# Kernel optimization log

Measured on AMD Instinct MI355X. Metric: run time of the kernel, lower is better.

The kernel has to match this reference:

```python
import jax, jax.numpy as jnp
import numpy as np

N_GRAPH = 1024
NODES_PER_GRAPH = 512
TOTAL_NODES = N_GRAPH * NODES_PER_GRAPH  # 524288
D_FEAT = 128
EPS = 1e-06


def setup_inputs() -> dict:
    key = jax.random.key(0)
    k1, k2, k3, k4 = jax.random.split(key, 4)
    x = jax.random.normal(k1, (TOTAL_NODES, D_FEAT), dtype=jnp.float32)
    # per-graph node counts; sum(n_node) == TOTAL_NODES (equal-size graphs)
    n_node = jnp.full((N_GRAPH,), NODES_PER_GRAPH, dtype=jnp.int32)
    mean_scale = jax.random.uniform(k2, (D_FEAT,), dtype=jnp.float32)
    scale = jax.random.uniform(k3, (D_FEAT,), dtype=jnp.float32)
    bias = jax.random.normal(k4, (D_FEAT,), dtype=jnp.float32)
    return {"x": x, "n_node": n_node, "mean_scale": mean_scale, "scale": scale, "bias": bias}


def reference(x, n_node, mean_scale, scale, bias):
    n_graph = n_node.shape[0]
    total_nodes = x.shape[0]
    node_graph_idx = jnp.repeat(jnp.arange(n_graph), n_node, axis=0,
                                total_repeat_length=total_nodes)  # [N]
    ones = jnp.ones((total_nodes, 1), dtype=x.dtype)
    counts = jax.ops.segment_sum(ones, node_graph_idx, n_graph)  # [G,1]
    # per-graph mean, broadcast back to nodes
    mean_g = jax.ops.segment_sum(x, node_graph_idx, n_graph) / counts  # [G,D]
    mean_n = jnp.repeat(mean_g, n_node, axis=0, total_repeat_length=total_nodes)
    # NOTE: faithful to source - the mean is scaled by mean_scale BEFORE both
    # the centering and the variance computation.
    mean_n = mean_n * mean_scale
    y = x - mean_n
    var_g = jax.ops.segment_sum((x - mean_n) ** 2, node_graph_idx, n_graph) / counts
    var_n = jnp.repeat(var_g, n_node, axis=0, total_repeat_length=total_nodes)
    mul = jax.lax.rsqrt(var_n + EPS) * scale
    y = y * mul + bias
    return y.astype(x.dtype)
```

## Files before the change

### kernel.cpp

```cpp
#include <hip/hip_runtime.h>

#define D_FEAT 128
#define F4 (D_FEAT / 4)
#define BLOCK 512
#define NSUB (BLOCK / F4)
#define EPS 1e-6f

typedef float nat4 __attribute__((ext_vector_type(4)));

__global__ __launch_bounds__(BLOCK, 8) void graphnorm_kernel(
    const float* __restrict__ x,
    const int* __restrict__ n_node,
    const float* __restrict__ mean_scale,
    const float* __restrict__ scale,
    const float* __restrict__ bias,
    float* __restrict__ y,
    int n_graph)
{
    const int g    = blockIdx.x;
    const int t    = threadIdx.x;
    const int lane = t & 63;
    const int wave = t >> 6;
    const int grp  = t & 31;
    const int nsub = t >> 5;

    __shared__ int    s_int[8];
    __shared__ float4 s_sum[8][32];
    __shared__ float4 s_sq [8][32];
    __shared__ float4 s_a[32];
    __shared__ float4 s_b[32];
    __shared__ int    s_off;

    int my = 0;
    for (int i = t; i < g; i += BLOCK) my += n_node[i];
    #pragma unroll
    for (int o = 32; o; o >>= 1) my += __shfl_down(my, o);
    if (lane == 0) s_int[wave] = my;
    __syncthreads();
    if (t == 0) {
        int tot = 0;
        #pragma unroll
        for (int w = 0; w < 8; w++) tot += s_int[w];
        s_off = tot;
    }
    __syncthreads();
    const int   node0 = s_off;
    const int   cnt   = n_node[g];
    const float inv   = 1.0f / (float)cnt;

    const float4* __restrict__ xg = (const float4*)x + (size_t)node0 * F4;
    float4*       __restrict__ yg = (float4*)y       + (size_t)node0 * F4;

    float4 sum = make_float4(0.f, 0.f, 0.f, 0.f);
    float4 sq  = make_float4(0.f, 0.f, 0.f, 0.f);

    #pragma unroll 4
    for (int node = nsub; node < cnt; node += NSUB) {
        float4 val = xg[(size_t)node * F4 + grp];
        sum.x += val.x; sum.y += val.y; sum.z += val.z; sum.w += val.w;
        sq.x  += val.x * val.x; sq.y += val.y * val.y;
        sq.z  += val.z * val.z; sq.w += val.w * val.w;
    }

    sum.x += __shfl_down(sum.x, 32); sum.y += __shfl_down(sum.y, 32);
    sum.z += __shfl_down(sum.z, 32); sum.w += __shfl_down(sum.w, 32);
    sq.x  += __shfl_down(sq.x, 32);  sq.y  += __shfl_down(sq.y, 32);
    sq.z  += __shfl_down(sq.z, 32);  sq.w  += __shfl_down(sq.w, 32);
    if (lane < 32) { s_sum[wave][lane] = sum; s_sq[wave][lane] = sq; }
    __syncthreads();

    if (t < 32) {
        float4 S = make_float4(0.f, 0.f, 0.f, 0.f);
        float4 Q = make_float4(0.f, 0.f, 0.f, 0.f);
        #pragma unroll
        for (int w = 0; w < 8; w++) {
            float4 a4 = s_sum[w][t];
            float4 b4 = s_sq[w][t];
            S.x += a4.x; S.y += a4.y; S.z += a4.z; S.w += a4.w;
            Q.x += b4.x; Q.y += b4.y; Q.z += b4.z; Q.w += b4.w;
        }
        const float4 ms = ((const float4*)mean_scale)[t];
        const float4 sc = ((const float4*)scale)[t];
        const float4 bs = ((const float4*)bias)[t];

        float4 A, B;
        {
            float mean = S.x * inv, m = mean * ms.x;
            float var  = Q.x * inv - 2.f * m * mean + m * m;
            A.x = rsqrtf(var + EPS) * sc.x; B.x = bs.x - m * A.x;
        }
        {
            float mean = S.y * inv, m = mean * ms.y;
            float var  = Q.y * inv - 2.f * m * mean + m * m;
            A.y = rsqrtf(var + EPS) * sc.y; B.y = bs.y - m * A.y;
        }
        {
            float mean = S.z * inv, m = mean * ms.z;
            float var  = Q.z * inv - 2.f * m * mean + m * m;
            A.z = rsqrtf(var + EPS) * sc.z; B.z = bs.z - m * A.z;
        }
        {
            float mean = S.w * inv, m = mean * ms.w;
            float var  = Q.w * inv - 2.f * m * mean + m * m;
            A.w = rsqrtf(var + EPS) * sc.w; B.w = bs.w - m * A.w;
        }
        s_a[t] = A; s_b[t] = B;
    }
    __syncthreads();

    const float4 a = s_a[grp];
    const float4 b = s_b[grp];

    #pragma unroll 4
    for (int node = nsub; node < cnt; node += NSUB) {
        float4 val = xg[(size_t)node * F4 + grp];
        nat4 r;
        r.x = val.x * a.x + b.x;
        r.y = val.y * a.y + b.y;
        r.z = val.z * a.z + b.z;
        r.w = val.w * a.w + b.w;
        __builtin_nontemporal_store(r, (nat4*)&yg[(size_t)node * F4 + grp]);
    }
}

extern "C" void kernel_launch(void* const* d_in, const int* in_sizes, int n_in,
                              void* d_out, int out_size, void* d_ws, size_t ws_size,
                              hipStream_t stream) {
    const float* x          = (const float*)d_in[0];
    const int*   n_node     = (const int*)d_in[1];
    const float* mean_scale = (const float*)d_in[2];
    const float* scale      = (const float*)d_in[3];
    const float* bias       = (const float*)d_in[4];
    float*       y          = (float*)d_out;

    const int n_graph = in_sizes[1];

    graphnorm_kernel<<<n_graph, BLOCK, 0, stream>>>(
        x, n_node, mean_scale, scale, bias, y, n_graph);
}
```

Measured before the change: 464.7 us.

## Keep whole graph tile in registers for single-pass normalize when count is 512

Adds a fast path for graphs with exactly 512 nodes. Each thread loads its 32 float4 values into registers once, computes the statistics, then reuses those registers for the output pass, so the second global read of x goes away. Launch bounds drop to one block per CU minimum to leave room for the 128 extra VGPRs. Occupancy falls, which may weaken latency hiding, and the general path stays for other node counts.

```diff
diff --git a/kernel.cpp b/kernel.cpp
--- a/kernel.cpp
+++ b/kernel.cpp
@@ -4,11 +4,13 @@
 #define F4 (D_FEAT / 4)
 #define BLOCK 512
 #define NSUB (BLOCK / F4)
+#define FAST_NODES 512
+#define PT (FAST_NODES * F4 / BLOCK)
 #define EPS 1e-6f
 
 typedef float nat4 __attribute__((ext_vector_type(4)));
 
-__global__ __launch_bounds__(BLOCK, 8) void graphnorm_kernel(
+__global__ __launch_bounds__(BLOCK, 1) void graphnorm_kernel(
     const float* __restrict__ x,
     const int* __restrict__ n_node,
     const float* __restrict__ mean_scale,
@@ -54,12 +56,29 @@
     float4 sum = make_float4(0.f, 0.f, 0.f, 0.f);
     float4 sq  = make_float4(0.f, 0.f, 0.f, 0.f);
 
-    #pragma unroll 4
-    for (int node = nsub; node < cnt; node += NSUB) {
-        float4 val = xg[(size_t)node * F4 + grp];
-        sum.x += val.x; sum.y += val.y; sum.z += val.z; sum.w += val.w;
-        sq.x  += val.x * val.x; sq.y += val.y * val.y;
-        sq.z  += val.z * val.z; sq.w += val.w * val.w;
+    const bool fast = (cnt == FAST_NODES);
+    float4 v[PT];
+
+    if (fast) {
+        const float4* __restrict__ p = xg + (size_t)nsub * F4 + grp;
+        #pragma unroll
+        for (int i = 0; i < PT; i++) {
+            v[i] = p[(size_t)i * (NSUB * F4)];
+        }
+        #pragma unroll
+        for (int i = 0; i < PT; i++) {
+            sum.x += v[i].x; sum.y += v[i].y; sum.z += v[i].z; sum.w += v[i].w;
+            sq.x  += v[i].x * v[i].x; sq.y += v[i].y * v[i].y;
+            sq.z  += v[i].z * v[i].z; sq.w += v[i].w * v[i].w;
+        }
+    } else {
+        #pragma unroll 4
+        for (int node = nsub; node < cnt; node += NSUB) {
+            float4 val = xg[(size_t)node * F4 + grp];
+            sum.x += val.x; sum.y += val.y; sum.z += val.z; sum.w += val.w;
+            sq.x  += val.x * val.x; sq.y += val.y * val.y;
+            sq.z  += val.z * val.z; sq.w += val.w * val.w;
+        }
     }
 
     sum.x += __shfl_down(sum.x, 32); sum.y += __shfl_down(sum.y, 32);
@@ -111,15 +130,28 @@
     const float4 a = s_a[grp];
     const float4 b = s_b[grp];
 
-    #pragma unroll 4
-    for (int node = nsub; node < cnt; node += NSUB) {
-        float4 val = xg[(size_t)node * F4 + grp];
-        nat4 r;
-        r.x = val.x * a.x + b.x;
-        r.y = val.y * a.y + b.y;
-        r.z = val.z * a.z + b.z;
-        r.w = val.w * a.w + b.w;
-        __builtin_nontemporal_store(r, (nat4*)&yg[(size_t)node * F4 + grp]);
+    if (fast) {
+        float4* __restrict__ q = yg + (size_t)nsub * F4 + grp;
+        #pragma unroll
+        for (int i = 0; i < PT; i++) {
+            nat4 r;
+            r.x = v[i].x * a.x + b.x;
+            r.y = v[i].y * a.y + b.y;
+            r.z = v[i].z * a.z + b.z;
+            r.w = v[i].w * a.w + b.w;
+            __builtin_nontemporal_store(r, (nat4*)&q[(size_t)i * (NSUB * F4)]);
+        }
+    } else {
+        #pragma unroll 4
+        for (int node = nsub; node < cnt; node += NSUB) {
+            float4 val = xg[(size_t)node * F4 + grp];
+            nat4 r;
+            r.x = val.x * a.x + b.x;
+            r.y = val.y * a.y + b.y;
+            r.z = val.z * a.z + b.z;
+            r.w = val.w * a.w + b.w;
+            __builtin_nontemporal_store(r, (nat4*)&yg[(size_t)node * F4 + grp]);
+        }
     }
 }
 
```

After: 451.5 us. 1.03x faster.
